# Performance work log

Hardware: AMD Instinct MI355X
Metric: run time of the kernel (lower is better)

The kernel has to match this reference:

```python
import jax, jax.numpy as jnp
import numpy as np

B, N, D = 1, 4096, 512
H, HD = 8, 64
NBINS = 512
CAND = 64
SCALE = 1.0 / np.sqrt(HD)
MAX_NORM = 1.0 - 1e-5
TWO_PI = 2.0 * np.pi


def _project(x):
    # Poincare-ball style projection: clip L2 norm of each point to MAX_NORM.
    n = jnp.sqrt(jnp.sum(x * x, axis=-1, keepdims=True))
    s = jnp.minimum(1.0, MAX_NORM / jnp.maximum(n, 1e-12))
    return x * s


def _bins(x):
    # Deterministic geometric binning (DavisCache stand-in): quantize the
    # angle of the first two coordinates into NBINS bins.
    ang = jnp.arctan2(x[..., 1], x[..., 0])  # (-pi, pi]
    b = jnp.floor((ang / TWO_PI + 0.5) * NBINS)
    return jnp.clip(b, 0, NBINS - 1).astype(jnp.int32)


def setup_inputs() -> dict:
    key0 = jax.random.key(0)
    ks = jax.random.split(key0, 12)
    w = 0.02  # typical init scale for projection weights
    return {
        "query": jax.random.normal(ks[0], (B, N, D), dtype=jnp.float32),
        "key": jax.random.normal(ks[1], (B, N, D), dtype=jnp.float32),
        "value": jax.random.normal(ks[2], (B, N, D), dtype=jnp.float32),
        "Wq": jax.random.normal(ks[3], (D, D), dtype=jnp.float32) * w,
        "bq": jnp.zeros((D,), dtype=jnp.float32),
        "Wk": jax.random.normal(ks[4], (D, D), dtype=jnp.float32) * w,
        "bk": jnp.zeros((D,), dtype=jnp.float32),
        "Wv": jax.random.normal(ks[5], (D, D), dtype=jnp.float32) * w,
        "bv": jnp.zeros((D,), dtype=jnp.float32),
        "Wo": jax.random.normal(ks[6], (D, D), dtype=jnp.float32) * w,
        "bo": jnp.zeros((D,), dtype=jnp.float32),
    }


def reference(query, key, value, Wq, bq, Wk, bk, Wv, bv, Wo, bo):
    Bq, Nq, Dm = query.shape
    Nk = key.shape[1]
    # projections + split heads -> (B, H, N, HD)
    q = (query @ Wq.T + bq).reshape(Bq, Nq, H, HD).transpose(0, 2, 1, 3)
    k = (key @ Wk.T + bk).reshape(Bq, Nk, H, HD).transpose(0, 2, 1, 3)
    v = (value @ Wv.T + bv).reshape(Bq, Nk, H, HD).transpose(0, 2, 1, 3)
    q = _project(q)
    k = _project(k)

    # geometric binning; candidate keys for a query are those whose bin is
    # within radius 1 of the query's bin (neighboring_bins, radius=1).
    qb = _bins(q)  # (B, H, Nq) int32
    kb = _bins(k)  # (B, H, Nk) int32
    mask = jnp.abs(qb[..., :, None] - kb[..., None, :]) <= 1  # (B,H,Nq,Nk)
    # fallback: if a query has no candidates, attend over all keys
    any_valid = jnp.any(mask, axis=-1, keepdims=True)
    eff = jnp.where(any_valid, mask, True)
    # keep only the first CAND candidates per query (by key index)
    rank = jnp.cumsum(eff.astype(jnp.int32), axis=-1) - 1
    sel = eff & (rank < CAND)

    scores = jnp.einsum("bhqd,bhkd->bhqk", q, k) * SCALE
    scores = jnp.where(sel, scores, -jnp.inf)
    attn = jax.nn.softmax(scores, axis=-1)  # dropout p=0.0 (eval mode)
    out = jnp.einsum("bhqk,bhkd->bhqd", attn, v)

    out = out.transpose(0, 2, 1, 3).reshape(Bq, Nq, Dm)
    return out @ Wo.T + bo
```

## Files before the change

kernel.cpp:

```cpp
#include <hip/hip_runtime.h>
#include <math.h>

typedef unsigned short u16;
typedef __attribute__((ext_vector_type(8))) short v8bf;
typedef __attribute__((ext_vector_type(4))) float f32x4;

#define N_TOK 4096
#define DMODEL 512
#define NHEAD 8
#define HDIM 64
#define CANDN 64
#define NBINS 512
#define BINCAP 64
#define QCAP 128
#define ATT_SCALE 0.125f
#define MAX_NORM_F 0.99999f

__device__ __forceinline__ float bf2f(u16 u) {
  union { unsigned int i; float f; } v; v.i = ((unsigned int)u) << 16; return v.f;
}
__device__ __forceinline__ u16 f2bf(float f) {
  union { float f; unsigned int i; } v; v.f = f;
  unsigned int x = v.i;
  return (u16)((x + 0x7fffu + ((x >> 16) & 1u)) >> 16);
}
__device__ __forceinline__ uint4 load_pack8(const float* __restrict__ p) {
  const float4 x0 = *(const float4*)p;
  const float4 x1 = *(const float4*)(p + 4);
  union { u16 h[8]; uint4 u; } r;
  r.h[0] = f2bf(x0.x); r.h[1] = f2bf(x0.y); r.h[2] = f2bf(x0.z); r.h[3] = f2bf(x0.w);
  r.h[4] = f2bf(x1.x); r.h[5] = f2bf(x1.y); r.h[6] = f2bf(x1.z); r.h[7] = f2bf(x1.w);
  return r.u;
}
__device__ __forceinline__ uint4 pack8v(const float4 x0, const float4 x1) {
  union { u16 h[8]; uint4 u; } r;
  r.h[0] = f2bf(x0.x); r.h[1] = f2bf(x0.y); r.h[2] = f2bf(x0.z); r.h[3] = f2bf(x0.w);
  r.h[4] = f2bf(x1.x); r.h[5] = f2bf(x1.y); r.h[6] = f2bf(x1.z); r.h[7] = f2bf(x1.w);
  return r.u;
}

__global__ __launch_bounds__(256) void prep_kernel(
    const float* __restrict__ query, const float* __restrict__ key_,
    const float* __restrict__ Wq, const float* __restrict__ Wk,
    const float* __restrict__ Wv, const float* __restrict__ Wo,
    u16* __restrict__ wqx, u16* __restrict__ wkx, u16* __restrict__ wvx,
    u16* __restrict__ wox,
    int* __restrict__ qb, int* __restrict__ kb, unsigned char* __restrict__ flags,
    int* __restrict__ khist)
{
  __shared__ float xs[16 * 516];
  const int blk = blockIdx.x;
  const int tid = threadIdx.x;

  if (blk >= 512) {
    const int u = ((blk - 512) << 8) + tid;
    if (u < 131072) {
      const int w = u >> 15;
      const int off = (u & 32767) << 3;
      const float* src = (w == 0) ? Wq : (w == 1) ? Wk : (w == 2) ? Wv : Wo;
      u16* dst = (w == 0) ? wqx : (w == 1) ? wkx : (w == 2) ? wvx : wox;
      *(uint4*)(dst + off) = load_pack8(src + off);
    } else if (u < 133120) {
      int4 z4; z4.x = 0; z4.y = 0; z4.z = 0; z4.w = 0;
      ((int4*)khist)[u - 131072] = z4;
    }
    return;
  }

  const int isk  = blk >> 8;
  const int tile = blk & 255;
  const float* X = isk ? key_ : query;
  const float* W = isk ? Wk : Wq;

#pragma unroll
  for (int i = 0; i < 8; ++i) {
    const int flat = i * 1024 + tid * 4;
    const int row = flat >> 9, col = flat & 511;
    *(float4*)&xs[row * 516 + col] = *(const float4*)(X + (tile * 16 + row) * DMODEL + col);
  }
  __syncthreads();

  const int n_local = tid >> 4;
  const int pair = tid & 15;
  const int h = pair >> 1, coord = pair & 1;
  const float* wrow = W + ((h << 6) + coord) * DMODEL;
  const float* xrow = &xs[n_local * 516];

  double c0 = 0.0, c1 = 0.0, c2 = 0.0, c3 = 0.0;
  for (int k = 0; k < DMODEL; k += 4) {
    const float4 xv = *(const float4*)(xrow + k);
    const float4 wv = *(const float4*)(wrow + k);
    c0 = fma((double)xv.x, (double)wv.x, c0);
    c1 = fma((double)xv.y, (double)wv.y, c1);
    c2 = fma((double)xv.z, (double)wv.z, c2);
    c3 = fma((double)xv.w, (double)wv.w, c3);
  }
  const double a = (c0 + c1) + (c2 + c3);
  const double other = __shfl_xor(a, 1);
  if (coord == 0) {
    const double a0 = a, a1 = other;
    const int n = tile * 16 + n_local;
    double ang = atan2(a1, a0);
    double t = (ang / 6.283185307179586 + 0.5) * 512.0;
    int b = (int)floor(t);
    b = b < 0 ? 0 : (b > 511 ? 511 : b);
    (isk ? kb : qb)[(h << 12) + n] = b;

    const double r = sqrt(a0 * a0 + a1 * a1);
    const double dist = fabs(t - nearbyint(t));
    const double margin = fmin(0.45, 3.3e-4 / fmax(r, 1e-30) + 5e-5);
    flags[(isk << 15) | (h << 12) | n] = (dist < margin) ? 1 : 0;
  }
}

__device__ float fdlibm_atanf(float x) {
#pragma clang fp contract(off)
  const float atanhi[4] = {4.6364760399e-01f, 7.8539812565e-01f,
                           9.8279368877e-01f, 1.5707962513e+00f};
  const float atanlo[4] = {5.0121582440e-09f, 3.7748947079e-08f,
                           3.4473217170e-08f, 7.5497894159e-08f};
  const float aT[5] = {3.3333328366e-01f, -1.9999158382e-01f, 1.4253635705e-01f,
                       -1.0648017377e-01f, 6.1687607318e-02f};
  unsigned ix = __float_as_uint(x);
  const unsigned sign = ix >> 31;
  ix &= 0x7fffffffu;
  int id;
  float z, w, s1, s2;
  if (ix >= 0x4c800000u) {
    z = atanhi[3] + 0x1p-120f;
    return sign ? -z : z;
  }
  if (ix < 0x3ee00000u) {
    if (ix < 0x39800000u) return x;
    id = -1;
  } else {
    x = fabsf(x);
    if (ix < 0x3f980000u) {
      if (ix < 0x3f300000u) { id = 0; x = (2.0f * x - 1.0f) / (2.0f + x); }
      else                  { id = 1; x = (x - 1.0f) / (x + 1.0f); }
    } else {
      if (ix < 0x401c0000u) { id = 2; x = (x - 1.5f) / (1.0f + 1.5f * x); }
      else                  { id = 3; x = -1.0f / x; }
    }
  }
  z = x * x;
  w = z * z;
  s1 = z * (aT[0] + w * (aT[2] + w * aT[4]));
  s2 = w * (aT[1] + w * aT[3]);
  if (id < 0) return x - x * (s1 + s2);
  z = atanhi[id] - ((x * (s1 + s2) - atanlo[id]) - x);
  return sign ? -z : z;
}

__device__ float fdlibm_atan2f(float y, float x) {
#pragma clang fp contract(off)
  const float pi = 3.1415927410e+00f, pi_lo = -8.7422776573e-08f;
  const unsigned hx = __float_as_uint(x), hy = __float_as_uint(y);
  if (hx == 0x3f800000u) return fdlibm_atanf(y);
  const unsigned m = ((hy >> 31) & 1u) | ((hx >> 30) & 2u);
  const unsigned ix = hx & 0x7fffffffu, iy = hy & 0x7fffffffu;
  if (iy == 0u) {
    switch (m) { case 0: case 1: return y; case 2: return pi; default: return -pi; }
  }
  if (ix == 0u) return (m & 1u) ? -1.57079637050628662f : 1.57079637050628662f;
  float z;
  if (ix + (26u << 23) < iy) {
    z = 1.57079637050628662f;
    return (m & 1u) ? -z : z;
  }
  if ((m & 2u) && iy + (26u << 23) < ix) z = 0.0f;
  else z = fdlibm_atanf(fabsf(y / x));
  switch (m) {
    case 0: return z;
    case 1: return -z;
    case 2: return pi - (z - pi_lo);
    default: return (z - pi_lo) - pi;
  }
}

__global__ __launch_bounds__(256) void binfix_kernel(
    const float* __restrict__ query, const float* __restrict__ key_,
    const float* __restrict__ Wq, const float* __restrict__ Wk,
    const unsigned char* __restrict__ flags,
    int* __restrict__ qb, int* __restrict__ kb)
{
  __shared__ int wle[64];
  __shared__ int wlc;

  const int tid = threadIdx.x;
  const int slice = blockIdx.x;

  if (tid == 0) wlc = 0;
  __syncthreads();
  if (tid < 128) {
    const int flat = (slice << 7) + tid;
    if (flags[flat]) {
      const int p = atomicAdd(&wlc, 1);
      if (p < 64) wle[p] = flat;
    }
  }
  __syncthreads();
  int nw = wlc; if (nw > 64) nw = 64;
  const int w = tid >> 6, d = tid & 63;
  for (int e = w; e < nw; e += 4) {
    const int flat = wle[e];
    const int n = flat & 4095;
    const int h = (flat >> 12) & 7;
    const int isk = flat >> 15;
    const float* xr = (isk ? key_ : query) + n * DMODEL;
    const float* wr = (isk ? Wk : Wq) + ((h << 6) + d) * DMODEL;
    float acc = 0.0f;
    for (int k = 0; k < DMODEL; k += 16) {
      const float4 xa = *(const float4*)(xr + k);
      const float4 xb = *(const float4*)(xr + k + 4);
      const float4 xc = *(const float4*)(xr + k + 8);
      const float4 xd = *(const float4*)(xr + k + 12);
      const float4 wa = *(const float4*)(wr + k);
      const float4 wb = *(const float4*)(wr + k + 4);
      const float4 wc = *(const float4*)(wr + k + 8);
      const float4 wd = *(const float4*)(wr + k + 12);
      acc = __fmaf_rn(xa.x, wa.x, acc); acc = __fmaf_rn(xa.y, wa.y, acc);
      acc = __fmaf_rn(xa.z, wa.z, acc); acc = __fmaf_rn(xa.w, wa.w, acc);
      acc = __fmaf_rn(xb.x, wb.x, acc); acc = __fmaf_rn(xb.y, wb.y, acc);
      acc = __fmaf_rn(xb.z, wb.z, acc); acc = __fmaf_rn(xb.w, wb.w, acc);
      acc = __fmaf_rn(xc.x, wc.x, acc); acc = __fmaf_rn(xc.y, wc.y, acc);
      acc = __fmaf_rn(xc.z, wc.z, acc); acc = __fmaf_rn(xc.w, wc.w, acc);
      acc = __fmaf_rn(xd.x, wd.x, acc); acc = __fmaf_rn(xd.y, wd.y, acc);
      acc = __fmaf_rn(xd.z, wd.z, acc); acc = __fmaf_rn(xd.w, wd.w, acc);
    }
    {
#pragma clang fp contract(off)
      const float sq = acc * acc;
      float rr[8];
#pragma unroll
      for (int j = 0; j < 8; ++j) rr[j] = __shfl(sq, j);
      for (int i = 8; i < 64; i += 8) {
#pragma unroll
        for (int j = 0; j < 8; ++j) rr[j] += __shfl(sq, i + j);
      }
      const float ss = ((rr[0] + rr[1]) + (rr[2] + rr[3])) +
                       ((rr[4] + rr[5]) + (rr[6] + rr[7]));
      const float nrm = __fsqrt_rn(ss);
      const float s = fminf(1.0f, 0.99999f / fmaxf(nrm, 1e-12f));
      const float c0 = __shfl(acc, 0) * s;
      const float c1 = __shfl(acc, 1) * s;
      const float cr = (float)atan2((double)c1, (double)c0);
      const float fd = fdlibm_atan2f(c1, c0);
      const float tol = fmaxf(fabsf(cr) * 6e-7f, 1e-30f);
      const float ang = (fabsf(fd - cr) <= tol) ? fd : cr;
      const float t = ((ang / 6.2831854820251465f) + 0.5f) * 512.0f;
      int b = (int)floorf(t);
      b = b < 0 ? 0 : (b > 511 ? 511 : b);
      if (d == 0) (isk ? kb : qb)[(h << 12) + n] = b;
    }
  }
}

__global__ __launch_bounds__(256) void gemm_qkv_kernel(
    const float* __restrict__ query, const float* __restrict__ key_,
    const float* __restrict__ value,
    const u16* __restrict__ wqx, const u16* __restrict__ wkx, const u16* __restrict__ wvx,
    const float* __restrict__ bq, const float* __restrict__ bk, const float* __restrict__ bv,
    u16* __restrict__ Qb, u16* __restrict__ Kb, u16* __restrict__ Vb)
{
  __shared__ u16 As[2][64 * 40];
  __shared__ u16 Ws[2][128 * 40];

  const int blk = blockIdx.x;
  const int tid = threadIdx.x;

  const int z = blk >> 8;
  const int rem = blk & 255;
  const int bm = (rem & 63) * 64;
  const int bn = (rem >> 6) * 128;

  const float* X  = (z == 0) ? query : (z == 1) ? key_ : value;
  const u16* W    = (z == 0) ? wqx : (z == 1) ? wkx : wvx;
  const float* bias = (z == 0) ? bq : (z == 1) ? bk : bv;
  u16* O          = (z == 0) ? Qb : (z == 1) ? Kb : Vb;

  const int lane = tid & 63;
  const int wave = tid >> 6;
  const int ra  = tid >> 2;
  const int oa  = (tid & 3) * 8;
  const int wm = (wave & 1) * 32;
  const int wn = (wave >> 1) * 64;
  const int l15 = lane & 15;
  const int quad = lane >> 4;

  f32x4 acc[2][4] = {};

  float4 a0f = *(const float4*)(X + (bm + ra) * DMODEL + oa);
  float4 a1f = *(const float4*)(X + (bm + ra) * DMODEL + oa + 4);
  uint4 w0 = *(const uint4*)(W + (bn + ra) * DMODEL + oa);
  uint4 w1 = *(const uint4*)(W + (bn + ra + 64) * DMODEL + oa);

  for (int kt = 0; kt < DMODEL; kt += 32) {
    const int p = (kt >> 5) & 1;
    *(uint4*)&As[p][ra * 40 + oa] = pack8v(a0f, a1f);
    *(uint4*)&Ws[p][ra * 40 + oa] = w0;
    *(uint4*)&Ws[p][(ra + 64) * 40 + oa] = w1;
    __syncthreads();
    if (kt + 32 < DMODEL) {
      a0f = *(const float4*)(X + (bm + ra) * DMODEL + kt + 32 + oa);
      a1f = *(const float4*)(X + (bm + ra) * DMODEL + kt + 32 + oa + 4);
      w0 = *(const uint4*)(W + (bn + ra) * DMODEL + kt + 32 + oa);
      w1 = *(const uint4*)(W + (bn + ra + 64) * DMODEL + kt + 32 + oa);
    }
    v8bf af[2], bfr[4];
#pragma unroll
    for (int i = 0; i < 2; ++i)
      af[i] = *(const v8bf*)&As[p][(wm + i * 16 + l15) * 40 + quad * 8];
#pragma unroll
    for (int j = 0; j < 4; ++j)
      bfr[j] = *(const v8bf*)&Ws[p][(wn + j * 16 + l15) * 40 + quad * 8];
#pragma unroll
    for (int i = 0; i < 2; ++i)
#pragma unroll
      for (int j = 0; j < 4; ++j)
        acc[i][j] = __builtin_amdgcn_mfma_f32_16x16x32_bf16(af[i], bfr[j], acc[i][j], 0, 0, 0);
  }

  float bval[4];
#pragma unroll
  for (int j = 0; j < 4; ++j) bval[j] = bias[bn + wn + j * 16 + l15];
  const int h = (bn + wn) >> 6;

#pragma unroll
  for (int i = 0; i < 2; ++i) {
#pragma unroll
    for (int r = 0; r < 4; ++r) {
      const int row = bm + wm + i * 16 + quad * 4 + r;
      float v0 = acc[i][0][r] + bval[0];
      float v1 = acc[i][1][r] + bval[1];
      float v2 = acc[i][2][r] + bval[2];
      float v3 = acc[i][3][r] + bval[3];
      if (z != 2) {
        float ss = v0 * v0 + v1 * v1 + v2 * v2 + v3 * v3;
#pragma unroll
        for (int o = 1; o < 16; o <<= 1) ss += __shfl_xor(ss, o);
        const float s = fminf(1.0f, MAX_NORM_F / fmaxf(sqrtf(ss), 1e-12f));
        v0 *= s; v1 *= s; v2 *= s; v3 *= s;
      }
      const int base = (((h << 12) + row) << 6) + l15;
      O[base +  0] = f2bf(v0); O[base + 16] = f2bf(v1);
      O[base + 32] = f2bf(v2); O[base + 48] = f2bf(v3);
    }
  }
}

__global__ __launch_bounds__(256) void bin_hist_kernel(
    const int* __restrict__ kb, const int* __restrict__ qb,
    int* __restrict__ khist, u16* __restrict__ blist,
    int* __restrict__ qhist, u16* __restrict__ qlist)
{
  const int h = blockIdx.x;
  const int type = blockIdx.y;
  const int* src = type ? qb : kb;
  int* hist = type ? qhist : khist;
  u16* list = type ? qlist : blist;
  const int cap = type ? QCAP : BINCAP;

  const int i = blockIdx.z * 256 + threadIdx.x;
  const int b = src[(h << 12) + i];
  const int pos = atomicAdd(&hist[(h << 9) + b], 1);
  if (pos < cap) list[((h << 9) + b) * cap + pos] = (u16)i;
}

__global__ __launch_bounds__(64) void attn_bin_kernel(
    const u16* __restrict__ Qb, const u16* __restrict__ Kb,
    const u16* __restrict__ Vb, const int* __restrict__ qhist,
    const u16* __restrict__ qlist, const int* __restrict__ khist,
    const u16* __restrict__ blist, u16* __restrict__ aout)
{
  __shared__ u16 kf[4 * 2 * 4 * 16 * 8];
  __shared__ u16 vf[4 * 2 * 4 * 16 * 8];
  __shared__ u16 pf[16 * 72];
  __shared__ u16 s_cand[64];
  __shared__ int s_qg[16];

  const int hb = blockIdx.x;
  const int h = hb >> 9;
  const int b = hb & 511;
  int qcnt = qhist[hb];
  if (qcnt > QCAP) qcnt = QCAP;
  if (qcnt == 0) return;

  const int lane = threadIdx.x;
  const int l15 = lane & 15;
  const int quad = lane >> 4;

  int v0 = 0xFFFF, v1 = 0xFFFF, v2 = 0xFFFF;
  int c0 = 0, c1 = 0, c2 = 0;
  if (b > 0) {
    c0 = khist[(h << 9) + b - 1];
    if (c0 > BINCAP) c0 = BINCAP;
    if (lane < c0) v0 = (int)blist[(((h << 9) + b - 1) << 6) + lane];
  }
  {
    c1 = khist[(h << 9) + b];
    if (c1 > BINCAP) c1 = BINCAP;
    if (lane < c1) v1 = (int)blist[(((h << 9) + b) << 6) + lane];
  }
  if (b < NBINS - 1) {
    c2 = khist[(h << 9) + b + 1];
    if (c2 > BINCAP) c2 = BINCAP;
    if (lane < c2) v2 = (int)blist[(((h << 9) + b + 1) << 6) + lane];
  }

  int r0 = 0, r1 = 0, r2 = 0;
#pragma unroll 8
  for (int j = 0; j < 64; ++j) {
    const int w0 = __shfl(v0, j);
    const int w1 = __shfl(v1, j);
    const int w2 = __shfl(v2, j);
    r0 += (w0 < v0) + (w1 < v0) + (w2 < v0);
    r1 += (w0 < v1) + (w1 < v1) + (w2 < v1);
    r2 += (w0 < v2) + (w1 < v2) + (w2 < v2);
  }
  const int tot = c0 + c1 + c2;
  const int ccnt = tot < CANDN ? tot : CANDN;
  const int ccnt_eff = (tot == 0) ? 64 : ccnt;
  if (tot == 0) {
    s_cand[lane] = (u16)lane;
  } else {
    if (v0 != 0xFFFF && r0 < CANDN) s_cand[r0] = (u16)v0;
    if (v1 != 0xFFFF && r1 < CANDN) s_cand[r1] = (u16)v1;
    if (v2 != 0xFFFF && r2 < CANDN) s_cand[r2] = (u16)v2;
  }
  __syncthreads();
  if (tot > 0 && lane >= ccnt) s_cand[lane] = s_cand[0];
  __syncthreads();

  {
    const int r = lane >> 3, s = lane & 7;
    const int ks = s >> 2, qd = s & 3;
#pragma unroll
    for (int it = 0; it < 8; ++it) {
      const int key = it * 8 + r;
      const int c = s_cand[key];
      const uint4 kv = *(const uint4*)(Kb + ((h << 18) | (c << 6)) + s * 8);
      const int idx = ((((key >> 4) * 2 + ks) * 4 + qd) * 16 + (key & 15)) * 8;
      *(uint4*)&kf[idx] = kv;
    }
  }
  {
    const int r = lane >> 3, s = lane & 7;
    const int nt = s >> 1, d0 = (s & 1) * 8;
#pragma unroll
    for (int it = 0; it < 8; ++it) {
      const int key = it * 8 + r;
      const int c = s_cand[key];
      union { u16 hh[8]; uint4 u; } vv;
      vv.u = *(const uint4*)(Vb + ((h << 18) | (c << 6)) + s * 8);
      const int kstep = key >> 5, qd = (key >> 3) & 3, j = key & 7;
#pragma unroll
      for (int m = 0; m < 8; ++m)
        vf[(((nt * 2 + kstep) * 4 + qd) * 16 + d0 + m) * 8 + j] = vv.hh[m];
    }
  }
  __syncthreads();

  v8bf akf[4][2], bvf[4][2];
#pragma unroll
  for (int t = 0; t < 4; ++t)
#pragma unroll
    for (int ks = 0; ks < 2; ++ks) {
      akf[t][ks] = *(const v8bf*)&kf[(((t * 2 + ks) * 4 + quad) * 16 + l15) * 8];
      bvf[t][ks] = *(const v8bf*)&vf[(((t * 2 + ks) * 4 + quad) * 16 + l15) * 8];
    }

  const int nchunk = (qcnt + 15) >> 4;
  for (int ci = 0; ci < nchunk; ++ci) {
    const int base = ci << 4;
    const int qcn = min(16, qcnt - base);
    __syncthreads();
    if (lane < 16) {
      int idx = base + lane;
      if (idx > qcnt - 1) idx = qcnt - 1;
      s_qg[lane] = (int)qlist[(hb << 7) + idx];
    }
    __syncthreads();

    const u16* qrow = Qb + ((h << 18) | (s_qg[l15] << 6));
    v8bf bq[2];
#pragma unroll
    for (int ks = 0; ks < 2; ++ks)
      bq[ks] = *(const v8bf*)(qrow + ks * 32 + quad * 8);

    float sc[16];
    __builtin_amdgcn_s_setprio(1);
#pragma unroll
    for (int t = 0; t < 4; ++t) {
      f32x4 sa = {0.f, 0.f, 0.f, 0.f};
      sa = __builtin_amdgcn_mfma_f32_16x16x32_bf16(akf[t][0], bq[0], sa, 0, 0, 0);
      sa = __builtin_amdgcn_mfma_f32_16x16x32_bf16(akf[t][1], bq[1], sa, 0, 0, 0);
#pragma unroll
      for (int r = 0; r < 4; ++r) {
        const int key = t * 16 + quad * 4 + r;
        sc[t * 4 + r] = (key < ccnt_eff) ? sa[r] * ATT_SCALE : -INFINITY;
      }
    }
    __builtin_amdgcn_s_setprio(0);
    float mx = sc[0];
#pragma unroll
    for (int i = 1; i < 16; ++i) mx = fmaxf(mx, sc[i]);
    mx = fmaxf(mx, __shfl_xor(mx, 16));
    mx = fmaxf(mx, __shfl_xor(mx, 32));
    float sum = 0.0f;
    float pe[16];
#pragma unroll
    for (int i = 0; i < 16; ++i) { pe[i] = __expf(sc[i] - mx); sum += pe[i]; }
    sum += __shfl_xor(sum, 16);
    sum += __shfl_xor(sum, 32);
    const float inv = 1.0f / sum;

    __syncthreads();
#pragma unroll
    for (int t = 0; t < 4; ++t)
#pragma unroll
      for (int r = 0; r < 4; ++r)
        pf[l15 * 72 + t * 16 + quad * 4 + r] = f2bf(pe[t * 4 + r] * inv);
    __syncthreads();

    v8bf ap[2];
#pragma unroll
    for (int ks = 0; ks < 2; ++ks)
      ap[ks] = *(const v8bf*)&pf[l15 * 72 + ks * 32 + quad * 8];

    __builtin_amdgcn_s_setprio(1);
#pragma unroll
    for (int nt = 0; nt < 4; ++nt) {
      f32x4 o = {0.f, 0.f, 0.f, 0.f};
      o = __builtin_amdgcn_mfma_f32_16x16x32_bf16(ap[0], bvf[nt][0], o, 0, 0, 0);
      o = __builtin_amdgcn_mfma_f32_16x16x32_bf16(ap[1], bvf[nt][1], o, 0, 0, 0);
#pragma unroll
      for (int r = 0; r < 4; ++r) {
        const int row = quad * 4 + r;
        if (row < qcn)
          aout[s_qg[row] * DMODEL + (h << 6) + nt * 16 + l15] = f2bf(o[r]);
      }
    }
    __builtin_amdgcn_s_setprio(0);
  }
}

__global__ __launch_bounds__(256) void gemm_out_kernel(
    const u16* __restrict__ A, const u16* __restrict__ W,
    const float* __restrict__ bias, float* __restrict__ O)
{
  __shared__ u16 As[2][64 * 40];
  __shared__ u16 Ws[2][64 * 40];

  const int tid  = threadIdx.x;
  const int lane = tid & 63;
  const int wave = tid >> 6;
  const int ra  = tid >> 2;
  const int oa  = (tid & 3) * 8;

  const int bm = blockIdx.x * 64;
  const int bn = blockIdx.y * 64;
  const int wm = (wave & 1) * 32;
  const int wn = (wave >> 1) * 32;
  const int l15 = lane & 15;
  const int quad = lane >> 4;

  f32x4 acc[2][2] = {};

  uint4 a0 = *(const uint4*)(A + (bm + ra) * DMODEL + oa);
  uint4 w0 = *(const uint4*)(W + (bn + ra) * DMODEL + oa);

  for (int kt = 0; kt < DMODEL; kt += 32) {
    const int p = (kt >> 5) & 1;
    *(uint4*)&As[p][ra * 40 + oa] = a0;
    *(uint4*)&Ws[p][ra * 40 + oa] = w0;
    __syncthreads();
    if (kt + 32 < DMODEL) {
      a0 = *(const uint4*)(A + (bm + ra) * DMODEL + kt + 32 + oa);
      w0 = *(const uint4*)(W + (bn + ra) * DMODEL + kt + 32 + oa);
    }
    v8bf af[2], bfr[2];
#pragma unroll
    for (int i = 0; i < 2; ++i)
      af[i] = *(const v8bf*)&As[p][(wm + i * 16 + l15) * 40 + quad * 8];
#pragma unroll
    for (int j = 0; j < 2; ++j)
      bfr[j] = *(const v8bf*)&Ws[p][(wn + j * 16 + l15) * 40 + quad * 8];
#pragma unroll
    for (int i = 0; i < 2; ++i)
#pragma unroll
      for (int j = 0; j < 2; ++j)
        acc[i][j] = __builtin_amdgcn_mfma_f32_16x16x32_bf16(af[i], bfr[j], acc[i][j], 0, 0, 0);
  }

#pragma unroll
  for (int j = 0; j < 2; ++j) {
    const int cg = bn + wn + j * 16 + l15;
    const float bval = bias[cg];
#pragma unroll
    for (int i = 0; i < 2; ++i) {
      const int rbase = bm + wm + i * 16 + quad * 4;
#pragma unroll
      for (int r = 0; r < 4; ++r)
        O[(rbase + r) * DMODEL + cg] = acc[i][j][r] + bval;
    }
  }
}

extern "C" void kernel_launch(void* const* d_in, const int* in_sizes, int n_in,
                              void* d_out, int out_size, void* d_ws, size_t ws_size,
                              hipStream_t stream) {
  const float* query = (const float*)d_in[0];
  const float* key_  = (const float*)d_in[1];
  const float* value = (const float*)d_in[2];
  const float* Wq = (const float*)d_in[3];
  const float* bq = (const float*)d_in[4];
  const float* Wk = (const float*)d_in[5];
  const float* bk = (const float*)d_in[6];
  const float* Wv = (const float*)d_in[7];
  const float* bv = (const float*)d_in[8];
  const float* Wo = (const float*)d_in[9];
  const float* bo = (const float*)d_in[10];

  char* ws = (char*)d_ws;
  u16* wqx   = (u16*)(ws + 12582912);
  u16* wkx   = (u16*)(ws + 13107200);
  u16* wvx   = (u16*)(ws + 13631488);
  u16* wox   = (u16*)(ws + 14155776);
  u16* Qb    = (u16*)(ws + 14680064);
  u16* Kb    = (u16*)(ws + 18874368);
  u16* Vb    = (u16*)(ws + 23068672);
  u16* aout  = (u16*)(ws + 27262976);
  int* qb    = (int*)(ws + 31457280);
  int* kb    = (int*)(ws + 31588352);
  unsigned char* flags = (unsigned char*)(ws + 31719424);
  int* khist = (int*)(ws + 31784960);
  int* qhist = (int*)(ws + 31801344);
  u16* blist = (u16*)(ws + 31817728);
  u16* qlist = (u16*)(ws + 32342016);

  prep_kernel<<<1032, 256, 0, stream>>>(
      query, key_, Wq, Wk, Wv, Wo,
      wqx, wkx, wvx, wox, qb, kb, flags, khist);
  binfix_kernel<<<512, 256, 0, stream>>>(
      query, key_, Wq, Wk, flags, qb, kb);
  gemm_qkv_kernel<<<768, 256, 0, stream>>>(
      query, key_, value, wqx, wkx, wvx, bq, bk, bv, Qb, Kb, Vb);
  bin_hist_kernel<<<dim3(8, 2, 16), 256, 0, stream>>>(
      kb, qb, khist, blist, qhist, qlist);
  attn_bin_kernel<<<4096, 64, 0, stream>>>(
      Qb, Kb, Vb, qhist, qlist, khist, blist, aout);
  gemm_out_kernel<<<dim3(64, 8), 256, 0, stream>>>(aout, wox, bo, (float*)d_out);
}
```

Baseline: 200.3 us.

## Fuse QKV GEMM into prep kernel and convert weights to bf16 on the fly

Removes the separate weight-conversion pass by loading fp32 weights directly in the QKV and output GEMMs and packing them to bf16 while staging to shared memory. The QKV GEMM blocks are merged into the prep kernel's grid, which drops one kernel launch and lets projection and bin computation run concurrently. In exchange, each GEMM block reads twice as many bytes of weights and does extra conversion work, and the shared-memory footprint is the union of both paths.

Result: no change. 200.7 us (+0.2%).

```diff
diff --git a/kernel.cpp b/kernel.cpp
--- a/kernel.cpp
+++ b/kernel.cpp
@@ -16,21 +16,10 @@
 #define ATT_SCALE 0.125f
 #define MAX_NORM_F 0.99999f
 
-__device__ __forceinline__ float bf2f(u16 u) {
-  union { unsigned int i; float f; } v; v.i = ((unsigned int)u) << 16; return v.f;
-}
 __device__ __forceinline__ u16 f2bf(float f) {
   union { float f; unsigned int i; } v; v.f = f;
   unsigned int x = v.i;
   return (u16)((x + 0x7fffu + ((x >> 16) & 1u)) >> 16);
-}
-__device__ __forceinline__ uint4 load_pack8(const float* __restrict__ p) {
-  const float4 x0 = *(const float4*)p;
-  const float4 x1 = *(const float4*)(p + 4);
-  union { u16 h[8]; uint4 u; } r;
-  r.h[0] = f2bf(x0.x); r.h[1] = f2bf(x0.y); r.h[2] = f2bf(x0.z); r.h[3] = f2bf(x0.w);
-  r.h[4] = f2bf(x1.x); r.h[5] = f2bf(x1.y); r.h[6] = f2bf(x1.z); r.h[7] = f2bf(x1.w);
-  return r.u;
 }
 __device__ __forceinline__ uint4 pack8v(const float4 x0, const float4 x1) {
   union { u16 h[8]; uint4 u; } r;
@@ -39,34 +28,119 @@
   return r.u;
 }
 
-__global__ __launch_bounds__(256) void prep_kernel(
+__global__ __launch_bounds__(256) void fused1_kernel(
     const float* __restrict__ query, const float* __restrict__ key_,
+    const float* __restrict__ value,
     const float* __restrict__ Wq, const float* __restrict__ Wk,
-    const float* __restrict__ Wv, const float* __restrict__ Wo,
-    u16* __restrict__ wqx, u16* __restrict__ wkx, u16* __restrict__ wvx,
-    u16* __restrict__ wox,
+    const float* __restrict__ Wv,
+    const float* __restrict__ bq, const float* __restrict__ bk,
+    const float* __restrict__ bv,
     int* __restrict__ qb, int* __restrict__ kb, unsigned char* __restrict__ flags,
-    int* __restrict__ khist)
+    int* __restrict__ khist,
+    u16* __restrict__ Qb, u16* __restrict__ Kb, u16* __restrict__ Vb)
 {
-  __shared__ float xs[16 * 516];
+  __shared__ __align__(16) char smem[33024];
   const int blk = blockIdx.x;
   const int tid = threadIdx.x;
 
+  if (blk >= 1280) {
+    int4 z4; z4.x = 0; z4.y = 0; z4.z = 0; z4.w = 0;
+#pragma unroll
+    for (int i = 0; i < 8; ++i) ((int4*)khist)[tid + i * 256] = z4;
+    return;
+  }
+
   if (blk >= 512) {
-    const int u = ((blk - 512) << 8) + tid;
-    if (u < 131072) {
-      const int w = u >> 15;
-      const int off = (u & 32767) << 3;
-      const float* src = (w == 0) ? Wq : (w == 1) ? Wk : (w == 2) ? Wv : Wo;
-      u16* dst = (w == 0) ? wqx : (w == 1) ? wkx : (w == 2) ? wvx : wox;
-      *(uint4*)(dst + off) = load_pack8(src + off);
-    } else if (u < 133120) {
-      int4 z4; z4.x = 0; z4.y = 0; z4.z = 0; z4.w = 0;
-      ((int4*)khist)[u - 131072] = z4;
+    u16* As = (u16*)smem;
+    u16* Ws = (u16*)(smem + 10240);
+
+    const int rel = blk - 512;
+    const int z = rel >> 8;
+    const int rem = rel & 255;
+    const int bm = (rem & 63) * 64;
+    const int bn = (rem >> 6) * 128;
+
+    const float* X  = (z == 0) ? query : (z == 1) ? key_ : value;
+    const float* WF = (z == 0) ? Wq : (z == 1) ? Wk : Wv;
+    const float* bias = (z == 0) ? bq : (z == 1) ? bk : bv;
+    u16* O          = (z == 0) ? Qb : (z == 1) ? Kb : Vb;
+
+    const int lane = tid & 63;
+    const int wave = tid >> 6;
+    const int ra  = tid >> 2;
+    const int oa  = (tid & 3) * 8;
+    const int wm = (wave & 1) * 32;
+    const int wn = (wave >> 1) * 64;
+    const int l15 = lane & 15;
+    const int quad = lane >> 4;
+
+    f32x4 acc[2][4] = {};
+
+    float4 a0f0 = *(const float4*)(X + (bm + ra) * DMODEL + oa);
+    float4 a0f1 = *(const float4*)(X + (bm + ra) * DMODEL + oa + 4);
+    float4 w0f0 = *(const float4*)(WF + (bn + ra) * DMODEL + oa);
+    float4 w0f1 = *(const float4*)(WF + (bn + ra) * DMODEL + oa + 4);
+    float4 w1f0 = *(const float4*)(WF + (bn + ra + 64) * DMODEL + oa);
+    float4 w1f1 = *(const float4*)(WF + (bn + ra + 64) * DMODEL + oa + 4);
+
+    for (int kt = 0; kt < DMODEL; kt += 32) {
+      const int p = (kt >> 5) & 1;
+      *(uint4*)&As[p * 2560 + ra * 40 + oa] = pack8v(a0f0, a0f1);
+      *(uint4*)&Ws[p * 5120 + ra * 40 + oa] = pack8v(w0f0, w0f1);
+      *(uint4*)&Ws[p * 5120 + (ra + 64) * 40 + oa] = pack8v(w1f0, w1f1);
+      __syncthreads();
+      if (kt + 32 < DMODEL) {
+        a0f0 = *(const float4*)(X + (bm + ra) * DMODEL + kt + 32 + oa);
+        a0f1 = *(const float4*)(X + (bm + ra) * DMODEL + kt + 32 + oa + 4);
+        w0f0 = *(const float4*)(WF + (bn + ra) * DMODEL + kt + 32 + oa);
+        w0f1 = *(const float4*)(WF + (bn + ra) * DMODEL + kt + 32 + oa + 4);
+        w1f0 = *(const float4*)(WF + (bn + ra + 64) * DMODEL + kt + 32 + oa);
+        w1f1 = *(const float4*)(WF + (bn + ra + 64) * DMODEL + kt + 32 + oa + 4);
+      }
+      v8bf af[2], bfr[4];
+#pragma unroll
+      for (int i = 0; i < 2; ++i)
+        af[i] = *(const v8bf*)&As[p * 2560 + (wm + i * 16 + l15) * 40 + quad * 8];
+#pragma unroll
+      for (int j = 0; j < 4; ++j)
+        bfr[j] = *(const v8bf*)&Ws[p * 5120 + (wn + j * 16 + l15) * 40 + quad * 8];
+#pragma unroll
+      for (int i = 0; i < 2; ++i)
+#pragma unroll
+        for (int j = 0; j < 4; ++j)
+          acc[i][j] = __builtin_amdgcn_mfma_f32_16x16x32_bf16(af[i], bfr[j], acc[i][j], 0, 0, 0);
+    }
+
+    float bval[4];
+#pragma unroll
+    for (int j = 0; j < 4; ++j) bval[j] = bias[bn + wn + j * 16 + l15];
+    const int h = (bn + wn) >> 6;
+
+#pragma unroll
+    for (int i = 0; i < 2; ++i) {
+#pragma unroll
+      for (int r = 0; r < 4; ++r) {
+        const int row = bm + wm + i * 16 + quad * 4 + r;
+        float v0 = acc[i][0][r] + bval[0];
+        float v1 = acc[i][1][r] + bval[1];
+        float v2 = acc[i][2][r] + bval[2];
+        float v3 = acc[i][3][r] + bval[3];
+        if (z != 2) {
+          float ss = v0 * v0 + v1 * v1 + v2 * v2 + v3 * v3;
+#pragma unroll
+          for (int o = 1; o < 16; o <<= 1) ss += __shfl_xor(ss, o);
+          const float s = fminf(1.0f, MAX_NORM_F / fmaxf(sqrtf(ss), 1e-12f));
+          v0 *= s; v1 *= s; v2 *= s; v3 *= s;
+        }
+        const int base = (((h << 12) + row) << 6) + l15;
+        O[base +  0] = f2bf(v0); O[base + 16] = f2bf(v1);
+        O[base + 32] = f2bf(v2); O[base + 48] = f2bf(v3);
+      }
     }
     return;
   }
 
+  float* xs = (float*)smem;
   const int isk  = blk >> 8;
   const int tile = blk & 255;
   const float* X = isk ? key_ : query;
@@ -256,99 +330,6 @@
   }
 }
 
-__global__ __launch_bounds__(256) void gemm_qkv_kernel(
-    const float* __restrict__ query, const float* __restrict__ key_,
-    const float* __restrict__ value,
-    const u16* __restrict__ wqx, const u16* __restrict__ wkx, const u16* __restrict__ wvx,
-    const float* __restrict__ bq, const float* __restrict__ bk, const float* __restrict__ bv,
-    u16* __restrict__ Qb, u16* __restrict__ Kb, u16* __restrict__ Vb)
-{
-  __shared__ u16 As[2][64 * 40];
-  __shared__ u16 Ws[2][128 * 40];
-
-  const int blk = blockIdx.x;
-  const int tid = threadIdx.x;
-
-  const int z = blk >> 8;
-  const int rem = blk & 255;
-  const int bm = (rem & 63) * 64;
-  const int bn = (rem >> 6) * 128;
-
-  const float* X  = (z == 0) ? query : (z == 1) ? key_ : value;
-  const u16* W    = (z == 0) ? wqx : (z == 1) ? wkx : wvx;
-  const float* bias = (z == 0) ? bq : (z == 1) ? bk : bv;
-  u16* O          = (z == 0) ? Qb : (z == 1) ? Kb : Vb;
-
-  const int lane = tid & 63;
-  const int wave = tid >> 6;
-  const int ra  = tid >> 2;
-  const int oa  = (tid & 3) * 8;
-  const int wm = (wave & 1) * 32;
-  const int wn = (wave >> 1) * 64;
-  const int l15 = lane & 15;
-  const int quad = lane >> 4;
-
-  f32x4 acc[2][4] = {};
-
-  float4 a0f = *(const float4*)(X + (bm + ra) * DMODEL + oa);
-  float4 a1f = *(const float4*)(X + (bm + ra) * DMODEL + oa + 4);
-  uint4 w0 = *(const uint4*)(W + (bn + ra) * DMODEL + oa);
-  uint4 w1 = *(const uint4*)(W + (bn + ra + 64) * DMODEL + oa);
-
-  for (int kt = 0; kt < DMODEL; kt += 32) {
-    const int p = (kt >> 5) & 1;
-    *(uint4*)&As[p][ra * 40 + oa] = pack8v(a0f, a1f);
-    *(uint4*)&Ws[p][ra * 40 + oa] = w0;
-    *(uint4*)&Ws[p][(ra + 64) * 40 + oa] = w1;
-    __syncthreads();
-    if (kt + 32 < DMODEL) {
-      a0f = *(const float4*)(X + (bm + ra) * DMODEL + kt + 32 + oa);
-      a1f = *(const float4*)(X + (bm + ra) * DMODEL + kt + 32 + oa + 4);
-      w0 = *(const uint4*)(W + (bn + ra) * DMODEL + kt + 32 + oa);
-      w1 = *(const uint4*)(W + (bn + ra + 64) * DMODEL + kt + 32 + oa);
-    }
-    v8bf af[2], bfr[4];
-#pragma unroll
-    for (int i = 0; i < 2; ++i)
-      af[i] = *(const v8bf*)&As[p][(wm + i * 16 + l15) * 40 + quad * 8];
-#pragma unroll
-    for (int j = 0; j < 4; ++j)
-      bfr[j] = *(const v8bf*)&Ws[p][(wn + j * 16 + l15) * 40 + quad * 8];
-#pragma unroll
-    for (int i = 0; i < 2; ++i)
-#pragma unroll
-      for (int j = 0; j < 4; ++j)
-        acc[i][j] = __builtin_amdgcn_mfma_f32_16x16x32_bf16(af[i], bfr[j], acc[i][j], 0, 0, 0);
-  }
-
-  float bval[4];
-#pragma unroll
-  for (int j = 0; j < 4; ++j) bval[j] = bias[bn + wn + j * 16 + l15];
-  const int h = (bn + wn) >> 6;
-
-#pragma unroll
-  for (int i = 0; i < 2; ++i) {
-#pragma unroll
-    for (int r = 0; r < 4; ++r) {
-      const int row = bm + wm + i * 16 + quad * 4 + r;
-      float v0 = acc[i][0][r] + bval[0];
-      float v1 = acc[i][1][r] + bval[1];
-      float v2 = acc[i][2][r] + bval[2];
-      float v3 = acc[i][3][r] + bval[3];
-      if (z != 2) {
-        float ss = v0 * v0 + v1 * v1 + v2 * v2 + v3 * v3;
-#pragma unroll
-        for (int o = 1; o < 16; o <<= 1) ss += __shfl_xor(ss, o);
-        const float s = fminf(1.0f, MAX_NORM_F / fmaxf(sqrtf(ss), 1e-12f));
-        v0 *= s; v1 *= s; v2 *= s; v3 *= s;
-      }
-      const int base = (((h << 12) + row) << 6) + l15;
-      O[base +  0] = f2bf(v0); O[base + 16] = f2bf(v1);
-      O[base + 32] = f2bf(v2); O[base + 48] = f2bf(v3);
-    }
-  }
-}
-
 __global__ __launch_bounds__(256) void bin_hist_kernel(
     const int* __restrict__ kb, const int* __restrict__ qb,
     int* __restrict__ khist, u16* __restrict__ blist,
@@ -546,7 +527,7 @@
 }
 
 __global__ __launch_bounds__(256) void gemm_out_kernel(
-    const u16* __restrict__ A, const u16* __restrict__ W,
+    const u16* __restrict__ A, const float* __restrict__ WF,
     const float* __restrict__ bias, float* __restrict__ O)
 {
   __shared__ u16 As[2][64 * 40];
@@ -568,16 +549,18 @@
   f32x4 acc[2][2] = {};
 
   uint4 a0 = *(const uint4*)(A + (bm + ra) * DMODEL + oa);
-  uint4 w0 = *(const uint4*)(W + (bn + ra) * DMODEL + oa);
+  float4 w0f0 = *(const float4*)(WF + (bn + ra) * DMODEL + oa);
+  float4 w0f1 = *(const float4*)(WF + (bn + ra) * DMODEL + oa + 4);
 
   for (int kt = 0; kt < DMODEL; kt += 32) {
     const int p = (kt >> 5) & 1;
     *(uint4*)&As[p][ra * 40 + oa] = a0;
-    *(uint4*)&Ws[p][ra * 40 + oa] = w0;
+    *(uint4*)&Ws[p][ra * 40 + oa] = pack8v(w0f0, w0f1);
     __syncthreads();
     if (kt + 32 < DMODEL) {
       a0 = *(const uint4*)(A + (bm + ra) * DMODEL + kt + 32 + oa);
-      w0 = *(const uint4*)(W + (bn + ra) * DMODEL + kt + 32 + oa);
+      w0f0 = *(const float4*)(WF + (bn + ra) * DMODEL + kt + 32 + oa);
+      w0f1 = *(const float4*)(WF + (bn + ra) * DMODEL + kt + 32 + oa + 4);
     }
     v8bf af[2], bfr[2];
 #pragma unroll
@@ -623,10 +606,6 @@
   const float* bo = (const float*)d_in[10];
 
   char* ws = (char*)d_ws;
-  u16* wqx   = (u16*)(ws + 12582912);
-  u16* wkx   = (u16*)(ws + 13107200);
-  u16* wvx   = (u16*)(ws + 13631488);
-  u16* wox   = (u16*)(ws + 14155776);
   u16* Qb    = (u16*)(ws + 14680064);
   u16* Kb    = (u16*)(ws + 18874368);
   u16* Vb    = (u16*)(ws + 23068672);
@@ -639,16 +618,14 @@
   u16* blist = (u16*)(ws + 31817728);
   u16* qlist = (u16*)(ws + 32342016);
 
-  prep_kernel<<<1032, 256, 0, stream>>>(
-      query, key_, Wq, Wk, Wv, Wo,
-      wqx, wkx, wvx, wox, qb, kb, flags, khist);
+  fused1_kernel<<<1281, 256, 0, stream>>>(
+      query, key_, value, Wq, Wk, Wv, bq, bk, bv,
+      qb, kb, flags, khist, Qb, Kb, Vb);
   binfix_kernel<<<512, 256, 0, stream>>>(
       query, key_, Wq, Wk, flags, qb, kb);
-  gemm_qkv_kernel<<<768, 256, 0, stream>>>(
-      query, key_, value, wqx, wkx, wvx, bq, bk, bv, Qb, Kb, Vb);
   bin_hist_kernel<<<dim3(8, 2, 16), 256, 0, stream>>>(
       kb, qb, khist, blist, qhist, qlist);
   attn_bin_kernel<<<4096, 64, 0, stream>>>(
       Qb, Kb, Vb, qhist, qlist, khist, blist, aout);
-  gemm_out_kernel<<<dim3(64, 8), 256, 0, stream>>>(aout, wox, bo, (float*)d_out);
-}
+  gemm_out_kernel<<<dim3(64, 8), 256, 0, stream>>>(aout, Wo, bo, (float*)d_out);
+}
```
